# Optimization experiments

Measured on AMD Instinct MI355X. Metric: run time of the kernel, lower is better.

## Reference

```python
import jax, jax.numpy as jnp
import numpy as np

BN_EPS = 1e-5
OUT_H, OUT_W = 32, 32  # crop_size / output_stride = 512/16


def setup_inputs() -> dict:
    key = jax.random.key(0)
    k1, k2, k3, k4 = jax.random.split(key, 4)
    x = jax.random.normal(k1, (16, 2048, 32, 32), dtype=jnp.float32)
    # conv1x1 weight, bias-free: [dim_out, dim_in]
    W = jax.random.normal(k2, (256, 2048), dtype=jnp.float32) * (1.0 / np.sqrt(2048.0))
    gamma = jax.random.normal(k3, (256,), dtype=jnp.float32) * 0.1 + 1.0
    beta = jax.random.normal(k4, (256,), dtype=jnp.float32) * 0.1
    return {"x": x, "W": W, "gamma": gamma, "beta": beta}


def reference(x, W, gamma, beta):
    # 1x1 conv, no bias: channel contraction
    y = jnp.einsum("nchw,oc->nohw", x, W)  # [N, dim_out, H, W]
    # BatchNorm2d in training mode: batch statistics over (N, H, W), biased var
    mean = jnp.mean(y, axis=(0, 2, 3), keepdims=True)
    var = jnp.mean(jnp.square(y - mean), axis=(0, 2, 3), keepdims=True)
    g = gamma.reshape(1, -1, 1, 1)
    b = beta.reshape(1, -1, 1, 1)
    y = g * (y - mean) * jax.lax.rsqrt(var + BN_EPS) + b
    # global average pool to 1x1
    pooled = jnp.mean(y, axis=(2, 3), keepdims=True)  # [N, dim_out, 1, 1]
    # adaptive avg pool from 1x1 to (OUT_H, OUT_W) is a pure broadcast
    out = jnp.broadcast_to(pooled, pooled.shape[:2] + (OUT_H, OUT_W))
    return out
```

## Files before the change

### kernel.cpp

```cpp
#include <hip/hip_runtime.h>
#include <hip/hip_bf16.h>
#include <stdint.h>

#define NB   16
#define CIN  2048
#define OUTC 256
#define HW   1024
#define BJ   64
#define BK   64
#define NJT  (HW / BJ)
#define KSTEPS (CIN / BK)

typedef __attribute__((ext_vector_type(8))) short bf16x8;
typedef __attribute__((ext_vector_type(4))) float f32x4;
typedef __attribute__((ext_vector_type(4))) unsigned int u32x4;

__device__ __forceinline__ unsigned int f2bf(float f) {
    union { float f; unsigned int u; } a; a.f = f;
    return (a.u + 0x7FFFu + ((a.u >> 16) & 1u)) >> 16;
}

__device__ __forceinline__ void block_sync_lds() {
    asm volatile("s_waitcnt lgkmcnt(0)" ::: "memory");
    __builtin_amdgcn_s_barrier();
    asm volatile("" ::: "memory");
}

__global__ void wprep_kernel(const float* __restrict__ W, unsigned short* __restrict__ Afrag) {
    int g  = blockIdx.x * blockDim.x + threadIdx.x;
    int o  = g >> 8;
    int kc = g & 255;
    const float4* p = reinterpret_cast<const float4*>(W + o * CIN + kc * 8);
    float4 v0 = p[0], v1 = p[1];
    u32x4 pk;
    pk.x = f2bf(v0.x) | (f2bf(v0.y) << 16);
    pk.y = f2bf(v0.z) | (f2bf(v0.w) << 16);
    pk.z = f2bf(v1.x) | (f2bf(v1.y) << 16);
    pk.w = f2bf(v1.z) | (f2bf(v1.w) << 16);
    int ks32 = kc >> 2, g8 = kc & 3;
    int lane = g8 * 16 + (o & 15), ot = o >> 4;
    *reinterpret_cast<u32x4*>(Afrag + (((size_t)ks32 * 16 + ot) * 64 + lane) * 8) = pk;
}

__global__ __launch_bounds__(512, 2) void gemm_stats_kernel(
    const float* __restrict__ x,
    const unsigned short* __restrict__ Afrag,
    float* __restrict__ s1_part,
    float* __restrict__ s2_part)
{
    __shared__ __align__(16) unsigned short B0[4096], B1[4096];
    __shared__ __align__(16) unsigned short PAD[40960];

    const int tid  = threadIdx.x;
    const int lane = tid & 63;
    const int wave = tid >> 6;
    const int blk  = blockIdx.x;
    const int n    = blk >> 4;
    const int jt   = blk & 15;
    const int j0   = jt * BJ;

    const float* xn = x + (size_t)n * CIN * HW;

    const int bj = tid & 63;
    const int kh = tid >> 6;
    const float* Bgp = xn + (size_t)(kh * 8) * HW + j0 + bj;
    const int offB = (kh >> 2) * 2048 + (bj >> 4) * 512 + (kh & 3) * 128 + (bj & 15) * 8;

    const int rbase = lane * 8;
    const unsigned short* Ab = Afrag + (size_t)lane * 8;

#define CLMP(v) (((v) < KSTEPS) ? (v) : KSTEPS - 1)
#define LDA(ks, R) { _Pragma("unroll") \
    for (int h = 0; h < 2; ++h) _Pragma("unroll") for (int t = 0; t < 2; ++t) \
        R[h * 2 + t] = *(const u32x4*)(Ab + ((((ks) * 2 + h) * 16 + 2 * wave + t) * 64) * 8); }
#define LDB(ks, F) { const float* p = Bgp + (size_t)(ks) * BK * HW; \
    _Pragma("unroll") for (int i = 0; i < 8; ++i) F[i] = p[(size_t)i * HW]; }
#define WRITEB(Bb, F) { u32x4 pk; \
    pk.x = f2bf(F[0]) | (f2bf(F[1]) << 16); pk.y = f2bf(F[2]) | (f2bf(F[3]) << 16); \
    pk.z = f2bf(F[4]) | (f2bf(F[5]) << 16); pk.w = f2bf(F[6]) | (f2bf(F[7]) << 16); \
    *(u32x4*)&Bb[offB] = pk; }
#define COMPUTE(Bb, R) { _Pragma("unroll") \
    for (int h = 0; h < 2; ++h) { \
        bf16x8 af0 = *(const bf16x8*)&R[h * 2 + 0]; \
        bf16x8 af1 = *(const bf16x8*)&R[h * 2 + 1]; \
        _Pragma("unroll") \
        for (int ni = 0; ni < 4; ++ni) { \
            bf16x8 bf = *(const bf16x8*)&Bb[h * 2048 + ni * 512 + rbase]; \
            acc[0][ni] = __builtin_amdgcn_mfma_f32_16x16x32_bf16(af0, bf, acc[0][ni], 0, 0, 0); \
            acc[1][ni] = __builtin_amdgcn_mfma_f32_16x16x32_bf16(af1, bf, acc[1][ni], 0, 0, 0); \
    } } }

    f32x4 acc[2][4] = {};
    u32x4 Aa0[4], Aa1[4];
    float BsA[8], BsB[8];

    LDA(0, Aa0); LDB(0, BsA);
    LDA(1, Aa1); LDB(1, BsB);
    WRITEB(B0, BsA);
    LDB(2, BsA);
    block_sync_lds();

    #pragma unroll 1
    for (int ks = 0; ks < KSTEPS; ks += 2) {
        COMPUTE(B0, Aa0);
        {
            LDA(CLMP(ks + 2), Aa0);
            WRITEB(B1, BsB);
            LDB(CLMP(ks + 3), BsB);
            block_sync_lds();
        }
        COMPUTE(B1, Aa1);
        {
            LDA(CLMP(ks + 3), Aa1);
        }
        if (ks + 2 < KSTEPS) {
            WRITEB(B0, BsA);
            LDB(CLMP(ks + 4), BsA);
            block_sync_lds();
        }
    }

    float rs[2][4], rq[2][4];
    #pragma unroll
    for (int mi = 0; mi < 2; ++mi)
        #pragma unroll
        for (int r = 0; r < 4; ++r) {
            float s = 0.f, q = 0.f;
            #pragma unroll
            for (int ni = 0; ni < 4; ++ni) {
                float v = acc[mi][ni][r];
                s += v; q += v * v;
            }
            rs[mi][r] = s; rq[mi][r] = q;
        }
    #pragma unroll
    for (int m = 1; m < 16; m <<= 1)
        #pragma unroll
        for (int mi = 0; mi < 2; ++mi)
            #pragma unroll
            for (int r = 0; r < 4; ++r) {
                rs[mi][r] += __shfl_xor(rs[mi][r], m, 64);
                rq[mi][r] += __shfl_xor(rq[mi][r], m, 64);
            }
    if ((lane & 15) == 0) {
        const int gK = lane >> 4;
        #pragma unroll
        for (int mi = 0; mi < 2; ++mi)
            #pragma unroll
            for (int r = 0; r < 4; ++r) {
                int o = wave * 32 + mi * 16 + gK * 4 + r;
                s1_part[(jt * NB + n) * OUTC + o] = rs[mi][r];
                s2_part[blk * OUTC + o]           = rq[mi][r];
            }
    }

    if (__builtin_expect((uintptr_t)x == 1, 0)) {
        PAD[tid] = (unsigned short)tid;
        __syncthreads();
        ((volatile unsigned short*)B0)[0] = PAD[(tid * 131) & 40959];
    }
#undef CLMP
#undef LDA
#undef LDB
#undef WRITEB
#undef COMPUTE
}

__global__ __launch_bounds__(256) void finalize_bcast_kernel(
    const float* __restrict__ s1_part,
    const float* __restrict__ s2_part,
    const float* __restrict__ gamma,
    const float* __restrict__ beta,
    float* __restrict__ out)
{
    const int tid   = threadIdx.x;
    const int slice = tid & 15;
    const int o_l   = tid >> 4;
    const int n0    = blockIdx.x >> 4;
    const int o     = (blockIdx.x & 15) * 16 + o_l;

    float S1 = 0.f, S2 = 0.f;
    #pragma unroll
    for (int q = 0; q < 16; ++q) {
        int p = slice * 16 + q;
        S1 += s1_part[p * OUTC + o];
        S2 += s2_part[p * OUTC + o];
    }
    float s1n = s1_part[(slice * NB + n0) * OUTC + o];
    #pragma unroll
    for (int m = 1; m < 16; m <<= 1) {
        S1  += __shfl_xor(S1, m, 64);
        S2  += __shfl_xor(S2, m, 64);
        s1n += __shfl_xor(s1n, m, 64);
    }
    float mean = S1 * (1.f / 16384.f);
    float var  = S2 * (1.f / 16384.f) - mean * mean;
    float inv  = rsqrtf(var + 1e-5f);
    float v = gamma[o] * (s1n * (1.f / 1024.f) - mean) * inv + beta[o];

    float4 vv = make_float4(v, v, v, v);
    float4* dst = reinterpret_cast<float4*>(out + ((size_t)(n0 * OUTC + o)) * HW);
    #pragma unroll
    for (int it = 0; it < 16; ++it)
        dst[it * 16 + slice] = vv;
}

extern "C" void kernel_launch(void* const* d_in, const int* in_sizes, int n_in,
                              void* d_out, int out_size, void* d_ws, size_t ws_size,
                              hipStream_t stream) {
    const float* x     = (const float*)d_in[0];
    const float* W     = (const float*)d_in[1];
    const float* gamma = (const float*)d_in[2];
    const float* beta  = (const float*)d_in[3];
    float* out = (float*)d_out;

    char* ws = (char*)d_ws;
    unsigned short* Afrag = (unsigned short*)ws;
    float* s1_part = (float*)(ws + (1 << 20));
    float* s2_part = (float*)(ws + (1 << 20) + (256 << 10));

    hipLaunchKernelGGL(wprep_kernel, dim3(256), dim3(256), 0, stream, W, Afrag);
    hipLaunchKernelGGL(gemm_stats_kernel, dim3(256), dim3(512), 0, stream,
                       x, Afrag, s1_part, s2_part);
    hipLaunchKernelGGL(finalize_bcast_kernel, dim3(NB * (OUTC / 16)), dim3(256), 0, stream,
                       s1_part, s2_part, gamma, beta, out);
}
```

Before: 47.75 us.

## Fuse weight bf16 prep into GEMM kernel with per-slice atomic flags

The separate weight-conversion kernel is removed. Each GEMM block now converts one of 64 K-slices of W into the bf16 fragment layout and publishes it with a fence and an atomic flag. Before loading A fragments, blocks spin on the 64 flags, which lets them start their first x loads early and drops one kernel launch. In exchange it adds a memset launch, a spin-wait that depends on all 256 blocks being co-resident, and cross-block synchronization overhead.

```diff
diff --git a/kernel.cpp b/kernel.cpp
--- a/kernel.cpp
+++ b/kernel.cpp
@@ -26,25 +26,11 @@
     asm volatile("" ::: "memory");
 }
 
-__global__ void wprep_kernel(const float* __restrict__ W, unsigned short* __restrict__ Afrag) {
-    int g  = blockIdx.x * blockDim.x + threadIdx.x;
-    int o  = g >> 8;
-    int kc = g & 255;
-    const float4* p = reinterpret_cast<const float4*>(W + o * CIN + kc * 8);
-    float4 v0 = p[0], v1 = p[1];
-    u32x4 pk;
-    pk.x = f2bf(v0.x) | (f2bf(v0.y) << 16);
-    pk.y = f2bf(v0.z) | (f2bf(v0.w) << 16);
-    pk.z = f2bf(v1.x) | (f2bf(v1.y) << 16);
-    pk.w = f2bf(v1.z) | (f2bf(v1.w) << 16);
-    int ks32 = kc >> 2, g8 = kc & 3;
-    int lane = g8 * 16 + (o & 15), ot = o >> 4;
-    *reinterpret_cast<u32x4*>(Afrag + (((size_t)ks32 * 16 + ot) * 64 + lane) * 8) = pk;
-}
-
 __global__ __launch_bounds__(512, 2) void gemm_stats_kernel(
     const float* __restrict__ x,
-    const unsigned short* __restrict__ Afrag,
+    const float* __restrict__ W,
+    unsigned short* __restrict__ Afrag,
+    unsigned int* __restrict__ flags,
     float* __restrict__ s1_part,
     float* __restrict__ s2_part)
 {
@@ -58,6 +44,28 @@
     const int n    = blk >> 4;
     const int jt   = blk & 15;
     const int j0   = jt * BJ;
+
+    {
+        const int s = blk & 63;
+        #pragma unroll
+        for (int half = 0; half < 2; ++half) {
+            int task = half * 512 + tid;
+            int ot = task >> 6;
+            int l  = task & 63;
+            const float4* p = reinterpret_cast<const float4*>(
+                W + (ot * 16 + (l & 15)) * CIN + 32 * s + (l >> 4) * 8);
+            float4 v0 = p[0], v1 = p[1];
+            u32x4 pk;
+            pk.x = f2bf(v0.x) | (f2bf(v0.y) << 16);
+            pk.y = f2bf(v0.z) | (f2bf(v0.w) << 16);
+            pk.z = f2bf(v1.x) | (f2bf(v1.y) << 16);
+            pk.w = f2bf(v1.z) | (f2bf(v1.w) << 16);
+            *reinterpret_cast<u32x4*>(Afrag + (((size_t)s * 16 + ot) * 64 + l) * 8) = pk;
+        }
+        __threadfence();
+        __syncthreads();
+        if (tid == 0) atomicAdd(&flags[s], 1u);
+    }
 
     const float* xn = x + (size_t)n * CIN * HW;
 
@@ -94,8 +102,17 @@
     u32x4 Aa0[4], Aa1[4];
     float BsA[8], BsB[8];
 
-    LDA(0, Aa0); LDB(0, BsA);
-    LDA(1, Aa1); LDB(1, BsB);
+    LDB(0, BsA);
+    LDB(1, BsB);
+    if (tid < 64) {
+        while (__hip_atomic_load(&flags[tid], __ATOMIC_RELAXED,
+                                 __HIP_MEMORY_SCOPE_AGENT) == 0u)
+            __builtin_amdgcn_s_sleep(2);
+    }
+    __syncthreads();
+    __threadfence();
+    LDA(0, Aa0);
+    LDA(1, Aa1);
     WRITEB(B0, BsA);
     LDB(2, BsA);
     block_sync_lds();
@@ -218,10 +235,11 @@
     unsigned short* Afrag = (unsigned short*)ws;
     float* s1_part = (float*)(ws + (1 << 20));
     float* s2_part = (float*)(ws + (1 << 20) + (256 << 10));
-
-    hipLaunchKernelGGL(wprep_kernel, dim3(256), dim3(256), 0, stream, W, Afrag);
+    unsigned int* flags = (unsigned int*)(ws + (1 << 20) + (512 << 10));
+
+    hipMemsetAsync(flags, 0, 64 * sizeof(unsigned int), stream);
     hipLaunchKernelGGL(gemm_stats_kernel, dim3(256), dim3(512), 0, stream,
-                       x, Afrag, s1_part, s2_part);
+                       x, W, Afrag, flags, s1_part, s2_part);
     hipLaunchKernelGGL(finalize_bcast_kernel, dim3(NB * (OUTC / 16)), dim3(256), 0, stream,
                        s1_part, s2_part, gamma, beta, out);
 }
```

Result: slower. 133.7 us (+180.0%).
